# Performance work log

Hardware: AMD Instinct MI355X
Metric: run time of the kernel (lower is better)

## Reference

```python
import jax, jax.numpy as jnp
import numpy as np

NEG = -1e9
BN_EPS = 1e-3  # keras BatchNormalization default epsilon
LRELU = 0.2    # GAT leaky-relu slope


def _gat(Xt, bias_mat, Wg, a1, a2, bg):
    """Dense multi-head GAT (Velickovic TF impl).
    Xt: [B,N,F], bias_mat: [B,N,N] additive mask (0 / -1e9).
    Wg: [H,F,D], a1/a2/bg: [H,D]. Returns [B,N,H*D]."""
    feats = jnp.einsum('bnf,hfd->bhnd', Xt, Wg)          # [B,H,N,D]
    f1 = jnp.einsum('bhnd,hd->bhn', feats, a1)
    f2 = jnp.einsum('bhnd,hd->bhn', feats, a2)
    logits = f1[:, :, :, None] + f2[:, :, None, :]        # [B,H,N,N]
    logits = jax.nn.leaky_relu(logits, LRELU) + bias_mat[:, None]
    coefs = jax.nn.softmax(logits, axis=-1)
    vals = jnp.einsum('bhnm,bhmd->bhnd', coefs, feats) + bg[None, :, None, :]
    vals = jax.nn.elu(vals)
    B, H, N, D = vals.shape
    return jnp.transpose(vals, (0, 2, 1, 3)).reshape(B, N, H * D)


def setup_inputs() -> dict:
    key = jax.random.key(0)
    ks = jax.random.split(key, 16)
    B, T, N, F = 4, 12, 2048, 64
    H, D = 4, 16           # attn_heads, hid_units
    C = H * D              # out_channels = 64

    X = jax.random.normal(ks[0], (B, T, N, F), dtype=jnp.float32)
    # random sparse adjacency (~avg degree 16) + self loops -> additive mask
    adj = jax.random.uniform(ks[1], (B, N, N)) < (16.0 / N)
    adj = adj | jnp.eye(N, dtype=bool)[None]
    bias_mat = jnp.where(adj, 0.0, NEG).astype(jnp.float32)

    he = lambda k, s: jax.random.normal(k, s, dtype=jnp.float32) * np.sqrt(2.0 / s[-2] if len(s) > 1 else 2.0 / s[-1])
    return {
        'X': X, 'bias_mat': bias_mat,
        'W_z': he(ks[2], (F, C)), 'Z_bias': he(ks[3], (1, C)),
        'W_h': he(ks[4], (F, C)), 'H_bias': he(ks[5], (1, C)),
        'Wg_z': he(ks[6], (H, F, D)), 'a1_z': he(ks[7], (H, D)),
        'a2_z': he(ks[8], (H, D)), 'bg_z': jnp.zeros((H, D), jnp.float32),
        'Wg_h': he(ks[9], (H, F, D)), 'a1_h': he(ks[10], (H, D)),
        'a2_h': he(ks[11], (H, D)), 'bg_h': jnp.zeros((H, D), jnp.float32),
        'bn_gamma': jnp.ones((C,), jnp.float32), 'bn_beta': jnp.zeros((C,), jnp.float32),
        'bn_mean': jnp.zeros((C,), jnp.float32), 'bn_var': jnp.ones((C,), jnp.float32),
    }


def reference(X, bias_mat, W_z, Z_bias, W_h, H_bias,
              Wg_z, a1_z, a2_z, bg_z, Wg_h, a1_h, a2_h, bg_h,
              bn_gamma, bn_beta, bn_mean, bn_var):
    B, T, N, F = X.shape
    C = W_z.shape[1]
    H0 = jnp.zeros((B, N, C), dtype=jnp.float32)

    def step(Hc, Xt):
        Z = _gat(Xt, bias_mat, Wg_z, a1_z, a2_z, bg_z) + Xt @ W_z + Z_bias + Hc
        Z = jax.nn.sigmoid(Z)
        Tt = _gat(Xt, bias_mat, Wg_h, a1_h, a2_h, bg_h) + Hc + Xt @ W_h + H_bias
        Tt = jnp.tanh(Tt)
        Hn = Z * Hc + (1.0 - Z) * Tt
        return Hn, None

    Xs = jnp.transpose(X, (1, 0, 2, 3))  # [T,B,N,F]
    Hf, _ = jax.lax.scan(step, H0, Xs)
    # last_layer=True path: BatchNorm (inference, moving stats) on final H
    out = (Hf - bn_mean) * jax.lax.rsqrt(bn_var + BN_EPS) * bn_gamma + bn_beta
    return out
```

## Files before the change

kernel.cpp:

```cpp
#include <hip/hip_runtime.h>
#include <cstdint>
#include <cstddef>

#define NB 4
#define NT 12
#define NN 2048
#define NF 64
#define NH 4
#define ND 16
#define NC 64
#define MAXD 64
#define NR (NB * NT * NN)

typedef _Float16 f16x8 __attribute__((ext_vector_type(8)));
typedef _Float16 f16x2 __attribute__((ext_vector_type(2)));
typedef float f32x4 __attribute__((ext_vector_type(4)));

#define LR(v) ((v) >= 0.f ? (v) : 0.2f * (v))
#define RCPF(x) __builtin_amdgcn_rcpf(x)

__global__ __launch_bounds__(256) void build_adj_k(const float* __restrict__ bias,
                                                   int* __restrict__ adj,
                                                   int* __restrict__ deg) {
  int gtid = blockIdx.x * 256 + threadIdx.x;
  int wid = gtid >> 6;
  int lane = threadIdx.x & 63;
  if (wid >= NB * NN) return;
  const float* row = bias + (size_t)wid * NN;
  int* arow = adj + (size_t)wid * MAXD;
  int count = 0;
  for (int c0 = 0; c0 < NN; c0 += 64) {
    float v = __builtin_nontemporal_load(row + c0 + lane);
    bool e = (v > -1e8f);
    unsigned long long m = __ballot(e);
    int pre = __popcll(m & ((1ull << lane) - 1ull));
    if (e) {
      int pos = count + pre;
      if (pos < MAXD) arow[pos] = c0 + lane;
    }
    count += __popcll(m);
  }
  if (lane == 0) deg[wid] = count < MAXD ? count : MAXD;
}

__global__ __launch_bounds__(256) void prep_w_k(
    const float* __restrict__ Wgz, const float* __restrict__ Wgh,
    const float* __restrict__ Wz,  const float* __restrict__ Wh,
    const float* __restrict__ a1z, const float* __restrict__ a2z,
    const float* __restrict__ a1h, const float* __restrict__ a2h,
    const float* __restrict__ Zb,  const float* __restrict__ Hb,
    _Float16* __restrict__ W16, float* __restrict__ biasC) {
  int idx = blockIdx.x * 256 + threadIdx.x;
  if (idx < 272 * 64) {
    int c = idx >> 6, k = idx & 63;
    float w;
    if (c < 64)       w = Wgz[((c >> 4) << 10) + (k << 4) + (c & 15)];
    else if (c < 128) { int q = c - 64; w = Wgh[((q >> 4) << 10) + (k << 4) + (q & 15)]; }
    else if (c < 192) w = Wz[(k << 6) + (c - 128)];
    else if (c < 256) w = Wh[(k << 6) + (c - 192)];
    else {
      int j = c - 256, h = j & 3;
      const float* Wg = (j & 4) ? Wgh : Wgz;
      const float* av = (j & 8) ? ((j & 4) ? a2h : a2z) : ((j & 4) ? a1h : a1z);
      float s = 0.f;
#pragma unroll
      for (int d = 0; d < 16; d++)
        s = fmaf(Wg[(h << 10) + (k << 4) + d], av[(h << 4) + d], s);
      w = s;
    }
    W16[idx] = (_Float16)w;
  }
  if (blockIdx.x == 0 && threadIdx.x < 128)
    biasC[threadIdx.x] =
        (threadIdx.x < 64) ? Zb[threadIdx.x] : Hb[threadIdx.x - 64];
}

__global__ __launch_bounds__(256) void mfma_gemm_k(
    const float* __restrict__ X, const _Float16* __restrict__ W16,
    const float* __restrict__ biasC,
    uint32_t* __restrict__ gbufF, uint32_t* __restrict__ gbufS,
    float* __restrict__ fbuf) {
  __shared__ uint32_t tr[4][16 * 68];
  const int tid = threadIdx.x;
  const int wv = tid >> 6, lane = tid & 63;
  const int m = lane & 15, quad = lane >> 4;
  const unsigned rw = blockIdx.x * 64 + wv * 16;
  uint32_t* tw = tr[wv];

  const float* xr = X + (size_t)(rw + m) * 64;
  float4 x0 = *(const float4*)(xr + quad * 8);
  float4 x1 = *(const float4*)(xr + quad * 8 + 4);
  float4 x2 = *(const float4*)(xr + 32 + quad * 8);
  float4 x3 = *(const float4*)(xr + 32 + quad * 8 + 4);
  f16x8 A0 = {(_Float16)x0.x, (_Float16)x0.y, (_Float16)x0.z, (_Float16)x0.w,
              (_Float16)x1.x, (_Float16)x1.y, (_Float16)x1.z, (_Float16)x1.w};
  f16x8 A1 = {(_Float16)x2.x, (_Float16)x2.y, (_Float16)x2.z, (_Float16)x2.w,
              (_Float16)x3.x, (_Float16)x3.y, (_Float16)x3.z, (_Float16)x3.w};

  float bzc[4], bhc[4];
#pragma unroll
  for (int j = 0; j < 4; j++) {
    bzc[j] = biasC[j * 16 + m];
    bhc[j] = biasC[64 + j * 16 + m];
  }
  const int rsub = lane >> 4, chk = lane & 15;

  f32x4 zacc[4], zs[4];
#pragma unroll
  for (int ct = 0; ct < 17; ct++) {
    const _Float16* wp = W16 + (ct * 16 + m) * 64;
    f16x8 B0 = *(const f16x8*)(wp + quad * 8);
    f16x8 B1 = *(const f16x8*)(wp + 32 + quad * 8);
    f32x4 acc = {0.f, 0.f, 0.f, 0.f};
    acc = __builtin_amdgcn_mfma_f32_16x16x32_f16(A0, B0, acc, 0, 0, 0);
    acc = __builtin_amdgcn_mfma_f32_16x16x32_f16(A1, B1, acc, 0, 0, 0);
    if (ct < 4) {
      zacc[ct] = acc;
    } else if (ct < 8) {
      const int j = ct - 4;
#pragma unroll
      for (int r = 0; r < 4; r++) {
        f16x2 pv = {(_Float16)zacc[j][r], (_Float16)acc[r]};
        tw[(quad * 4 + r) * 68 + j * 16 + m] = __builtin_bit_cast(uint32_t, pv);
      }
      if (ct == 7) {
#pragma unroll
        for (int i = 0; i < 4; i++) {
          int row = i * 4 + rsub;
          uint4 v = *(const uint4*)&tw[row * 68 + chk * 4];
          *(uint4*)&gbufF[(size_t)(rw + row) * 64 + chk * 4] = v;
        }
      }
    } else if (ct < 12) {
#pragma unroll
      for (int r = 0; r < 4; r++) zs[ct - 8][r] = acc[r] + bzc[ct - 8];
    } else if (ct < 16) {
      const int j = ct - 12;
#pragma unroll
      for (int r = 0; r < 4; r++) {
        f16x2 pv = {(_Float16)zs[j][r], (_Float16)(acc[r] + bhc[j])};
        tw[(quad * 4 + r) * 68 + j * 16 + m] = __builtin_bit_cast(uint32_t, pv);
      }
      if (ct == 15) {
#pragma unroll
        for (int i = 0; i < 4; i++) {
          int row = i * 4 + rsub;
          uint4 v = *(const uint4*)&tw[row * 68 + chk * 4];
          *(uint4*)&gbufS[(size_t)(rw + row) * 64 + chk * 4] = v;
        }
      }
    } else {
      const unsigned rb = rw + quad * 4;
#pragma unroll
      for (int r = 0; r < 4; r++) fbuf[(size_t)(rb + r) * 16 + m] = acc[r];
    }
  }
}

__global__ __launch_bounds__(256) void attn_k(
    const uint32_t* __restrict__ gbufF, const uint32_t* __restrict__ gbufS,
    const float* __restrict__ fbuf,
    const int* __restrict__ adj, const int* __restrict__ deg,
    const float* __restrict__ bgz, const float* __restrict__ bgh,
    uint32_t* __restrict__ abuf) {
  __shared__ int adjL[4][MAXD];
  __shared__ float wexp[4][8][68];
  const int tid = threadIdx.x;
  const int lane = tid & 63;
  const int ws = tid >> 6;
  const int node = blockIdx.x * 4 + ws;
  const int t = blockIdx.y;
  const int b = node >> 11;
  const int nl = node & (NN - 1);
  const int dg = deg[node];
  adjL[ws][lane] = (lane < dg) ? adj[node * MAXD + lane] : 0;
  const int dgp = (dg + 7) & ~7;

  const unsigned rb = (unsigned)(b * NT + t) * NN;
  const float* fb = fbuf + (size_t)rb * 16;
  const uint32_t* gF = gbufF + (size_t)rb * 64;
  const uint32_t* gS = gbufS + (size_t)rb * 64;
  const int ch = lane, hh = lane >> 4;

  {
    const float4* p = (const float4*)(fb + nl * 16);
    float4 f1z = p[0], f1h = p[1];
    if (lane < dg) {
      int mm = adjL[ws][lane];
      const float4* q = (const float4*)(fb + mm * 16);
      float4 f2z = q[2], f2h = q[3];
      wexp[ws][0][lane] = __expf(LR(f1z.x + f2z.x));
      wexp[ws][1][lane] = __expf(LR(f1z.y + f2z.y));
      wexp[ws][2][lane] = __expf(LR(f1z.z + f2z.z));
      wexp[ws][3][lane] = __expf(LR(f1z.w + f2z.w));
      wexp[ws][4][lane] = __expf(LR(f1h.x + f2h.x));
      wexp[ws][5][lane] = __expf(LR(f1h.y + f2h.y));
      wexp[ws][6][lane] = __expf(LR(f1h.z + f2h.z));
      wexp[ws][7][lane] = __expf(LR(f1h.w + f2h.w));
    } else {
#pragma unroll
      for (int k = 0; k < 8; k++) wexp[ws][k][lane] = 0.f;
    }
  }

  float az = 0.f, ah = 0.f, sz = 0.f, sh = 0.f;
  const float* wz = wexp[ws][hh];
  const float* wh = wexp[ws][4 + hh];
  for (int mi = 0; mi < dgp; mi += 8) {
    int4 ma = *(const int4*)&adjL[ws][mi];
    int4 mb = *(const int4*)&adjL[ws][mi + 4];
    float4 wza = *(const float4*)&wz[mi];
    float4 wzb = *(const float4*)&wz[mi + 4];
    float4 wha = *(const float4*)&wh[mi];
    float4 whb = *(const float4*)&wh[mi + 4];
    uint32_t d0 = gF[(ma.x << 6) + ch];
    uint32_t d1 = gF[(ma.y << 6) + ch];
    uint32_t d2 = gF[(ma.z << 6) + ch];
    uint32_t d3 = gF[(ma.w << 6) + ch];
    uint32_t d4 = gF[(mb.x << 6) + ch];
    uint32_t d5 = gF[(mb.y << 6) + ch];
    uint32_t d6 = gF[(mb.z << 6) + ch];
    uint32_t d7 = gF[(mb.w << 6) + ch];
    f16x2 p0 = __builtin_bit_cast(f16x2, d0);
    f16x2 p1 = __builtin_bit_cast(f16x2, d1);
    f16x2 p2 = __builtin_bit_cast(f16x2, d2);
    f16x2 p3 = __builtin_bit_cast(f16x2, d3);
    f16x2 p4 = __builtin_bit_cast(f16x2, d4);
    f16x2 p5 = __builtin_bit_cast(f16x2, d5);
    f16x2 p6 = __builtin_bit_cast(f16x2, d6);
    f16x2 p7 = __builtin_bit_cast(f16x2, d7);
    az = fmaf(wza.x, (float)p0.x, az); ah = fmaf(wha.x, (float)p0.y, ah);
    az = fmaf(wza.y, (float)p1.x, az); ah = fmaf(wha.y, (float)p1.y, ah);
    az = fmaf(wza.z, (float)p2.x, az); ah = fmaf(wha.z, (float)p2.y, ah);
    az = fmaf(wza.w, (float)p3.x, az); ah = fmaf(wha.w, (float)p3.y, ah);
    az = fmaf(wzb.x, (float)p4.x, az); ah = fmaf(whb.x, (float)p4.y, ah);
    az = fmaf(wzb.y, (float)p5.x, az); ah = fmaf(whb.y, (float)p5.y, ah);
    az = fmaf(wzb.z, (float)p6.x, az); ah = fmaf(whb.z, (float)p6.y, ah);
    az = fmaf(wzb.w, (float)p7.x, az); ah = fmaf(whb.w, (float)p7.y, ah);
    sz += (wza.x + wza.y) + (wza.z + wza.w) + (wzb.x + wzb.y) + (wzb.z + wzb.w);
    sh += (wha.x + wha.y) + (wha.z + wha.w) + (whb.x + whb.y) + (whb.z + whb.w);
  }
  az *= RCPF(sz);
  ah *= RCPF(sh);

  f16x2 sp = __builtin_bit_cast(f16x2, gS[(nl << 6) + ch]);
  float vz = az + bgz[ch]; vz = vz > 0.f ? vz : __expf(vz) - 1.f;
  float vh = ah + bgh[ch]; vh = vh > 0.f ? vh : __expf(vh) - 1.f;
  f16x2 pre = {(_Float16)(vz + (float)sp.x), (_Float16)(vh + (float)sp.y)};
  abuf[(size_t)(rb + nl) * 64 + ch] = __builtin_bit_cast(uint32_t, pre);
}

__global__ __launch_bounds__(256) void gru_k(
    const uint32_t* __restrict__ abuf,
    const float* __restrict__ gam, const float* __restrict__ bet,
    const float* __restrict__ mu, const float* __restrict__ var,
    float* __restrict__ out) {
  const int gtid = blockIdx.x * 256 + threadIdx.x;
  const int node = gtid >> 6, ch = gtid & 63;
  const int b = node >> 11, nl = node & (NN - 1);
  float hc = 0.f;
#pragma unroll
  for (int t = 0; t < NT; t++) {
    f16x2 pre = __builtin_bit_cast(
        f16x2, abuf[(size_t)((b * NT + t) * NN + nl) * 64 + ch]);
    float zg = RCPF(1.f + __expf(-((float)pre.x + hc)));
    float ta = (float)pre.y + hc;
    float tg = 1.f - 2.f * RCPF(__expf(2.f * ta) + 1.f);
    hc = zg * hc + (1.f - zg) * tg;
  }
  out[gtid] = (hc - mu[ch]) * rsqrtf(var[ch] + 1e-3f) * gam[ch] + bet[ch];
}

extern "C" void kernel_launch(void* const* d_in, const int* in_sizes, int n_in,
                              void* d_out, int out_size, void* d_ws, size_t ws_size,
                              hipStream_t stream) {
  (void)in_sizes; (void)n_in; (void)out_size; (void)ws_size;
  const float* X   = (const float*)d_in[0];
  const float* bm  = (const float*)d_in[1];
  const float* Wz  = (const float*)d_in[2];
  const float* Zb  = (const float*)d_in[3];
  const float* Wh  = (const float*)d_in[4];
  const float* Hb  = (const float*)d_in[5];
  const float* Wgz = (const float*)d_in[6];
  const float* a1z = (const float*)d_in[7];
  const float* a2z = (const float*)d_in[8];
  const float* bgz = (const float*)d_in[9];
  const float* Wgh = (const float*)d_in[10];
  const float* a1h = (const float*)d_in[11];
  const float* a2h = (const float*)d_in[12];
  const float* bgh = (const float*)d_in[13];
  const float* gam = (const float*)d_in[14];
  const float* bet = (const float*)d_in[15];
  const float* mu  = (const float*)d_in[16];
  const float* var = (const float*)d_in[17];
  float* out = (float*)d_out;

  char* p = (char*)d_ws;
  uint32_t* gbufF = (uint32_t*)p; p += (size_t)NR * 64 * sizeof(uint32_t);
  uint32_t* gbufS = (uint32_t*)p; p += (size_t)NR * 64 * sizeof(uint32_t);
  float*    fbuf  = (float*)p;    p += (size_t)NR * 16 * sizeof(float);
  uint32_t* abuf  = (uint32_t*)p; p += (size_t)NR * 64 * sizeof(uint32_t);
  int*      adj   = (int*)p;      p += (size_t)NB * NN * MAXD * sizeof(int);
  int*      deg   = (int*)p;      p += (size_t)NB * NN * sizeof(int);
  _Float16* W16   = (_Float16*)p; p += 272 * 64 * sizeof(_Float16);
  float*    biasC = (float*)p;    p += 128 * sizeof(float);

  prep_w_k<<<dim3(68), dim3(256), 0, stream>>>(
      Wgz, Wgh, Wz, Wh, a1z, a2z, a1h, a2h, Zb, Hb, W16, biasC);
  build_adj_k<<<dim3(NB * NN / 4), dim3(256), 0, stream>>>(bm, adj, deg);
  mfma_gemm_k<<<dim3(NR / 64), dim3(256), 0, stream>>>(
      X, W16, biasC, gbufF, gbufS, fbuf);
  attn_k<<<dim3(NB * NN / 4, NT), dim3(256), 0, stream>>>(
      gbufF, gbufS, fbuf, adj, deg, bgz, bgh, abuf);
  gru_k<<<dim3(NB * NN * 64 / 256), dim3(256), 0, stream>>>(
      abuf, gam, bet, mu, var, out);
}
```

Measured before the change: 249.6 us.

## Fuse attention and GRU kernels, looping timesteps per node with fma_mix

```diff
diff --git a/kernel.cpp b/kernel.cpp
--- a/kernel.cpp
+++ b/kernel.cpp
@@ -18,6 +18,13 @@
 
 #define LR(v) ((v) >= 0.f ? (v) : 0.2f * (v))
 #define RCPF(x) __builtin_amdgcn_rcpf(x)
+
+#define MACLO(acc, w, d)                                                      \
+  asm("v_fma_mix_f32 %0, %1, %2, %0 op_sel:[0,0,0] op_sel_hi:[0,1,0]"         \
+      : "+v"(acc) : "v"(w), "v"(d))
+#define MACHI(acc, w, d)                                                      \
+  asm("v_fma_mix_f32 %0, %1, %2, %0 op_sel:[0,1,0] op_sel_hi:[0,1,0]"         \
+      : "+v"(acc) : "v"(w), "v"(d))
 
 __global__ __launch_bounds__(256) void build_adj_k(const float* __restrict__ bias,
                                                    int* __restrict__ adj,
@@ -157,118 +164,102 @@
   }
 }
 
-__global__ __launch_bounds__(256) void attn_k(
+__global__ __launch_bounds__(256) void attn_gru_k(
     const uint32_t* __restrict__ gbufF, const uint32_t* __restrict__ gbufS,
     const float* __restrict__ fbuf,
     const int* __restrict__ adj, const int* __restrict__ deg,
     const float* __restrict__ bgz, const float* __restrict__ bgh,
-    uint32_t* __restrict__ abuf) {
+    const float* __restrict__ gam, const float* __restrict__ bet,
+    const float* __restrict__ mu, const float* __restrict__ var,
+    float* __restrict__ out) {
   __shared__ int adjL[4][MAXD];
   __shared__ float wexp[4][8][68];
   const int tid = threadIdx.x;
   const int lane = tid & 63;
   const int ws = tid >> 6;
   const int node = blockIdx.x * 4 + ws;
-  const int t = blockIdx.y;
   const int b = node >> 11;
   const int nl = node & (NN - 1);
   const int dg = deg[node];
   adjL[ws][lane] = (lane < dg) ? adj[node * MAXD + lane] : 0;
-  const int dgp = (dg + 7) & ~7;
-
-  const unsigned rb = (unsigned)(b * NT + t) * NN;
-  const float* fb = fbuf + (size_t)rb * 16;
-  const uint32_t* gF = gbufF + (size_t)rb * 64;
-  const uint32_t* gS = gbufS + (size_t)rb * 64;
+  const int dgp = (dg + 3) & ~3;
   const int ch = lane, hh = lane >> 4;
-
-  {
-    const float4* p = (const float4*)(fb + nl * 16);
-    float4 f1z = p[0], f1h = p[1];
-    if (lane < dg) {
-      int mm = adjL[ws][lane];
-      const float4* q = (const float4*)(fb + mm * 16);
-      float4 f2z = q[2], f2h = q[3];
-      wexp[ws][0][lane] = __expf(LR(f1z.x + f2z.x));
-      wexp[ws][1][lane] = __expf(LR(f1z.y + f2z.y));
-      wexp[ws][2][lane] = __expf(LR(f1z.z + f2z.z));
-      wexp[ws][3][lane] = __expf(LR(f1z.w + f2z.w));
-      wexp[ws][4][lane] = __expf(LR(f1h.x + f2h.x));
-      wexp[ws][5][lane] = __expf(LR(f1h.y + f2h.y));
-      wexp[ws][6][lane] = __expf(LR(f1h.z + f2h.z));
-      wexp[ws][7][lane] = __expf(LR(f1h.w + f2h.w));
-    } else {
-#pragma unroll
-      for (int k = 0; k < 8; k++) wexp[ws][k][lane] = 0.f;
-    }
-  }
-
-  float az = 0.f, ah = 0.f, sz = 0.f, sh = 0.f;
-  const float* wz = wexp[ws][hh];
-  const float* wh = wexp[ws][4 + hh];
-  for (int mi = 0; mi < dgp; mi += 8) {
-    int4 ma = *(const int4*)&adjL[ws][mi];
-    int4 mb = *(const int4*)&adjL[ws][mi + 4];
-    float4 wza = *(const float4*)&wz[mi];
-    float4 wzb = *(const float4*)&wz[mi + 4];
-    float4 wha = *(const float4*)&wh[mi];
-    float4 whb = *(const float4*)&wh[mi + 4];
-    uint32_t d0 = gF[(ma.x << 6) + ch];
-    uint32_t d1 = gF[(ma.y << 6) + ch];
-    uint32_t d2 = gF[(ma.z << 6) + ch];
-    uint32_t d3 = gF[(ma.w << 6) + ch];
-    uint32_t d4 = gF[(mb.x << 6) + ch];
-    uint32_t d5 = gF[(mb.y << 6) + ch];
-    uint32_t d6 = gF[(mb.z << 6) + ch];
-    uint32_t d7 = gF[(mb.w << 6) + ch];
-    f16x2 p0 = __builtin_bit_cast(f16x2, d0);
-    f16x2 p1 = __builtin_bit_cast(f16x2, d1);
-    f16x2 p2 = __builtin_bit_cast(f16x2, d2);
-    f16x2 p3 = __builtin_bit_cast(f16x2, d3);
-    f16x2 p4 = __builtin_bit_cast(f16x2, d4);
-    f16x2 p5 = __builtin_bit_cast(f16x2, d5);
-    f16x2 p6 = __builtin_bit_cast(f16x2, d6);
-    f16x2 p7 = __builtin_bit_cast(f16x2, d7);
-    az = fmaf(wza.x, (float)p0.x, az); ah = fmaf(wha.x, (float)p0.y, ah);
-    az = fmaf(wza.y, (float)p1.x, az); ah = fmaf(wha.y, (float)p1.y, ah);
-    az = fmaf(wza.z, (float)p2.x, az); ah = fmaf(wha.z, (float)p2.y, ah);
-    az = fmaf(wza.w, (float)p3.x, az); ah = fmaf(wha.w, (float)p3.y, ah);
-    az = fmaf(wzb.x, (float)p4.x, az); ah = fmaf(whb.x, (float)p4.y, ah);
-    az = fmaf(wzb.y, (float)p5.x, az); ah = fmaf(whb.y, (float)p5.y, ah);
-    az = fmaf(wzb.z, (float)p6.x, az); ah = fmaf(whb.z, (float)p6.y, ah);
-    az = fmaf(wzb.w, (float)p7.x, az); ah = fmaf(whb.w, (float)p7.y, ah);
-    sz += (wza.x + wza.y) + (wza.z + wza.w) + (wzb.x + wzb.y) + (wzb.z + wzb.w);
-    sh += (wha.x + wha.y) + (wha.z + wha.w) + (whb.x + whb.y) + (whb.z + whb.w);
-  }
-  az *= RCPF(sz);
-  ah *= RCPF(sh);
-
-  f16x2 sp = __builtin_bit_cast(f16x2, gS[(nl << 6) + ch]);
-  float vz = az + bgz[ch]; vz = vz > 0.f ? vz : __expf(vz) - 1.f;
-  float vh = ah + bgh[ch]; vh = vh > 0.f ? vh : __expf(vh) - 1.f;
-  f16x2 pre = {(_Float16)(vz + (float)sp.x), (_Float16)(vh + (float)sp.y)};
-  abuf[(size_t)(rb + nl) * 64 + ch] = __builtin_bit_cast(uint32_t, pre);
-}
-
-__global__ __launch_bounds__(256) void gru_k(
-    const uint32_t* __restrict__ abuf,
-    const float* __restrict__ gam, const float* __restrict__ bet,
-    const float* __restrict__ mu, const float* __restrict__ var,
-    float* __restrict__ out) {
-  const int gtid = blockIdx.x * 256 + threadIdx.x;
-  const int node = gtid >> 6, ch = gtid & 63;
-  const int b = node >> 11, nl = node & (NN - 1);
+  const int sr = lane & 7, ss = lane >> 3;
+
+#pragma unroll
+  for (int k = 0; k < 8; k++) wexp[ws][k][lane] = 0.f;
+
+  const float bz = bgz[ch], bh = bgh[ch];
+  const float bnm = mu[ch];
+  const float bns = rsqrtf(var[ch] + 1e-3f);
+  const float bng = gam[ch], bnb = bet[ch];
+
   float hc = 0.f;
-#pragma unroll
+#pragma unroll 1
   for (int t = 0; t < NT; t++) {
-    f16x2 pre = __builtin_bit_cast(
-        f16x2, abuf[(size_t)((b * NT + t) * NN + nl) * 64 + ch]);
-    float zg = RCPF(1.f + __expf(-((float)pre.x + hc)));
-    float ta = (float)pre.y + hc;
-    float tg = 1.f - 2.f * RCPF(__expf(2.f * ta) + 1.f);
+    const unsigned rb = (unsigned)(b * NT + t) * NN;
+    const float* fb = fbuf + (size_t)rb * 16;
+    const uint32_t* gF = gbufF + (size_t)rb * 64;
+    const uint32_t* gS = gbufS + (size_t)rb * 64;
+
+    {
+      const float4* p = (const float4*)(fb + nl * 16);
+      float4 f1z = p[0], f1h = p[1];
+      if (lane < dg) {
+        int mm = adjL[ws][lane];
+        const float4* q = (const float4*)(fb + mm * 16);
+        float4 f2z = q[2], f2h = q[3];
+        wexp[ws][0][lane] = __expf(LR(f1z.x + f2z.x));
+        wexp[ws][1][lane] = __expf(LR(f1z.y + f2z.y));
+        wexp[ws][2][lane] = __expf(LR(f1z.z + f2z.z));
+        wexp[ws][3][lane] = __expf(LR(f1z.w + f2z.w));
+        wexp[ws][4][lane] = __expf(LR(f1h.x + f2h.x));
+        wexp[ws][5][lane] = __expf(LR(f1h.y + f2h.y));
+        wexp[ws][6][lane] = __expf(LR(f1h.z + f2h.z));
+        wexp[ws][7][lane] = __expf(LR(f1h.w + f2h.w));
+      }
+    }
+
+    float4 u0 = *(const float4*)&wexp[ws][sr][ss * 8];
+    float4 u1 = *(const float4*)&wexp[ws][sr][ss * 8 + 4];
+    float part = ((u0.x + u0.y) + (u0.z + u0.w)) +
+                 ((u1.x + u1.y) + (u1.z + u1.w));
+    part += __shfl_xor(part, 8);
+    part += __shfl_xor(part, 16);
+    part += __shfl_xor(part, 32);
+    const float rsz = RCPF(__shfl(part, hh));
+    const float rsh = RCPF(__shfl(part, 4 + hh));
+
+    float az = 0.f, ah = 0.f;
+    const float* wz = wexp[ws][hh];
+    const float* wh = wexp[ws][4 + hh];
+    for (int mi = 0; mi < dgp; mi += 4) {
+      int4 ma = *(const int4*)&adjL[ws][mi];
+      float4 wza = *(const float4*)&wz[mi];
+      float4 wha = *(const float4*)&wh[mi];
+      uint32_t d0 = gF[(ma.x << 6) + ch];
+      uint32_t d1 = gF[(ma.y << 6) + ch];
+      uint32_t d2 = gF[(ma.z << 6) + ch];
+      uint32_t d3 = gF[(ma.w << 6) + ch];
+      MACLO(az, wza.x, d0); MACHI(ah, wha.x, d0);
+      MACLO(az, wza.y, d1); MACHI(ah, wha.y, d1);
+      MACLO(az, wza.z, d2); MACHI(ah, wha.z, d2);
+      MACLO(az, wza.w, d3); MACHI(ah, wha.w, d3);
+    }
+    az *= rsz;
+    ah *= rsh;
+
+    f16x2 sp = __builtin_bit_cast(f16x2, gS[(nl << 6) + ch]);
+    float vz = az + bz; vz = vz > 0.f ? vz : __expf(vz) - 1.f;
+    float vh = ah + bh; vh = vh > 0.f ? vh : __expf(vh) - 1.f;
+    float zp = vz + (float)sp.x + hc;
+    float tp = vh + (float)sp.y + hc;
+    float zg = RCPF(1.f + __expf(-zp));
+    float tg = 1.f - 2.f * RCPF(__expf(2.f * tp) + 1.f);
     hc = zg * hc + (1.f - zg) * tg;
   }
-  out[gtid] = (hc - mu[ch]) * rsqrtf(var[ch] + 1e-3f) * gam[ch] + bet[ch];
+
+  out[(size_t)node * 64 + ch] = (hc - bnm) * bns * bng + bnb;
 }
 
 extern "C" void kernel_launch(void* const* d_in, const int* in_sizes, int n_in,
@@ -299,7 +290,6 @@
   uint32_t* gbufF = (uint32_t*)p; p += (size_t)NR * 64 * sizeof(uint32_t);
   uint32_t* gbufS = (uint32_t*)p; p += (size_t)NR * 64 * sizeof(uint32_t);
   float*    fbuf  = (float*)p;    p += (size_t)NR * 16 * sizeof(float);
-  uint32_t* abuf  = (uint32_t*)p; p += (size_t)NR * 64 * sizeof(uint32_t);
   int*      adj   = (int*)p;      p += (size_t)NB * NN * MAXD * sizeof(int);
   int*      deg   = (int*)p;      p += (size_t)NB * NN * sizeof(int);
   _Float16* W16   = (_Float16*)p; p += 272 * 64 * sizeof(_Float16);
@@ -310,8 +300,6 @@
   build_adj_k<<<dim3(NB * NN / 4), dim3(256), 0, stream>>>(bm, adj, deg);
   mfma_gemm_k<<<dim3(NR / 64), dim3(256), 0, stream>>>(
       X, W16, biasC, gbufF, gbufS, fbuf);
-  attn_k<<<dim3(NB * NN / 4, NT), dim3(256), 0, stream>>>(
-      gbufF, gbufS, fbuf, adj, deg, bgz, bgh, abuf);
-  gru_k<<<dim3(NB * NN * 64 / 256), dim3(256), 0, stream>>>(
-      abuf, gam, bet, mu, var, out);
-}
+  attn_gru_k<<<dim3(NB * NN / 4), dim3(256), 0, stream>>>(
+      gbufF, gbufS, fbuf, adj, deg, bgz, bgh, gam, bet, mu, var, out);
+}
```

Result: faster. 243.2 us (-2.5%).
